# Kernel tuning notes

Hardware: AMD Instinct MI355X
Metric: run time of the kernel (lower is better)

## Reference

```python
import jax, jax.numpy as jnp
import numpy as np

TEMPERATURE_F = 0.5  # temperature_f from __init__


def setup_inputs() -> dict:
    key = jax.random.key(0)
    k1, k2 = jax.random.split(key)
    B, D = 4096, 512
    h_i = jax.random.normal(k1, (B, D), dtype=jnp.float32)
    h_j = jax.random.normal(k2, (B, D), dtype=jnp.float32)
    return {"h_i": h_i, "h_j": h_j}


def reference(h_i, h_j) -> jnp.ndarray:
    # NT-Xent loss (forward_private). N = 2*batch_size.
    B = h_i.shape[0]
    N = 2 * B
    h = jnp.concatenate([h_i, h_j], axis=0)          # [N, D]
    sim = (h @ h.T) / TEMPERATURE_F                   # [N, N]

    # Positive pairs: sim[i, i+B] and sim[i+B, i]
    sim_i_j = jnp.diagonal(sim, offset=B)             # [B]
    sim_j_i = jnp.diagonal(sim, offset=-B)            # [B]
    pos = jnp.concatenate([sim_i_j, sim_j_i], axis=0)  # [N]

    # Original builds logits = [pos | negatives] where negatives are the row of
    # sim with the diagonal and the positive entry removed, and labels are 0.
    # Cross-entropy per row = -pos_i + logsumexp(pos_i, negatives_i)
    #                       = -pos_i + logsumexp over row i of sim excluding the
    #                         diagonal (the positive entry equals pos_i, so the
    #                         set of logsumexp'd values is identical).
    neg_inf = jnp.finfo(sim.dtype).min
    diag = jnp.eye(N, dtype=bool)
    sim_masked = jnp.where(diag, neg_inf, sim)        # exclude self-similarity
    lse = jax.nn.logsumexp(sim_masked, axis=1)        # [N]

    loss = jnp.sum(lse - pos) / N                     # CE sum reduction, / N
    return loss
```

## Files before the change

### kernel.cpp

```cpp
#include <hip/hip_runtime.h>
#include <hip/hip_bf16.h>
#include <float.h>

#define BN_ 4096
#define DD  512
#define NN  8192
#define SCALE 2.0f

typedef unsigned short u16;
typedef __attribute__((ext_vector_type(8))) short short8;
typedef __attribute__((ext_vector_type(4))) float floatx4;

struct alignas(8) U16x4 { u16 x, y, z, w; };

__device__ __forceinline__ u16 f2bf(float f) {
    union { float f; unsigned u; } c; c.f = f;
    unsigned u = c.u;
    unsigned r = (u + 0x7fffu + ((u >> 16) & 1u)) >> 16;
    return (u16)r;
}

__device__ __forceinline__ void async_copy16(const u16* g, u16* l) {
    __builtin_amdgcn_global_load_lds(
        (const __attribute__((address_space(1))) void*)g,
        (__attribute__((address_space(3))) void*)l, 16, 0, 0);
}

__global__ __launch_bounds__(256) void convert_pos_kernel(const float* __restrict__ hi,
                                                          const float* __restrict__ hj,
                                                          u16* __restrict__ H,
                                                          float* __restrict__ Pos,
                                                          float* __restrict__ out) {
    __shared__ float red[4];
    int t = blockIdx.x * 256 + threadIdx.x;
    int e = t * 4;
    const int BD = BN_ * DD;
    float4 a = *(const float4*)(hi + e);
    float4 b = *(const float4*)(hj + e);
    U16x4 oa, ob;
    oa.x = f2bf(a.x); oa.y = f2bf(a.y); oa.z = f2bf(a.z); oa.w = f2bf(a.w);
    ob.x = f2bf(b.x); ob.y = f2bf(b.y); ob.z = f2bf(b.z); ob.w = f2bf(b.w);
    *(U16x4*)(H + e) = oa;
    *(U16x4*)(H + BD + e) = ob;
    float dot = a.x * b.x + a.y * b.y + a.z * b.z + a.w * b.w;
#pragma unroll
    for (int msk = 1; msk < 64; msk <<= 1) dot += __shfl_xor(dot, msk);
    int lane = threadIdx.x & 63, wid = threadIdx.x >> 6;
    if (lane == 0) red[wid] = dot;
    __syncthreads();
    if (threadIdx.x == 0) {
        Pos[blockIdx.x] = red[0] + red[1] + red[2] + red[3];
        if (blockIdx.x == 0) *out = 0.0f;
    }
}

__global__ __launch_bounds__(256, 3) void gram_kernel(const u16* __restrict__ H,
                                                      float* __restrict__ Mpart,
                                                      float* __restrict__ Spart) {
    __shared__ u16 As[128 * 64];
    __shared__ u16 Bs[128 * 64];
    __shared__ float Rm[2][128], Rs[2][128];
    __shared__ float Cm[2][128], Cs[2][128];

    const int tid  = threadIdx.x;
    const int lane = tid & 63;
    const int wid  = tid >> 6;
    const int quad = lane >> 4;
    const int ln15 = lane & 15;
    const int wr = wid >> 1, wc = wid & 1;

    int t = blockIdx.x;
    int bi = (int)((sqrtf(8.0f * (float)t + 1.0f) - 1.0f) * 0.5f);
    while ((bi + 1) * (bi + 2) / 2 <= t) bi++;
    while (bi * (bi + 1) / 2 > t) bi--;
    const int bj = t - bi * (bi + 1) / 2;
    const bool diag = (bi == bj);
    const int biBase = bi * 128, bjBase = bj * 128;

    const u16* srcA[4];
    int ldsOff[4];
#pragma unroll
    for (int j = 0; j < 4; j++) {
        int c   = j * 256 + tid;
        int row = c >> 3;
        int kc  = (c & 7) ^ (row & 7);
        srcA[j]   = H + (size_t)(biBase + row) * DD + kc * 8;
        ldsOff[j] = c * 8;
    }
    const ptrdiff_t dB = (ptrdiff_t)(bjBase - biBase) * DD;

    floatx4 acc[4][4];
#pragma unroll
    for (int i = 0; i < 4; i++)
#pragma unroll
        for (int j = 0; j < 4; j++) acc[i][j] = (floatx4)0.0f;

    for (int k0 = 0; k0 < DD; k0 += 64) {
#pragma unroll
        for (int j = 0; j < 4; j++) async_copy16(srcA[j] + k0,      &As[ldsOff[j]]);
#pragma unroll
        for (int j = 0; j < 4; j++) async_copy16(srcA[j] + dB + k0, &Bs[ldsOff[j]]);
        __syncthreads();

#pragma unroll
        for (int kk = 0; kk < 2; kk++) {
            int ck = kk * 4 + quad;
            short8 a[4], b[4];
#pragma unroll
            for (int tm = 0; tm < 4; tm++) {
                int r = wr * 64 + tm * 16 + ln15;
                a[tm] = *(const short8*)&As[(r * 8 + (ck ^ (r & 7))) * 8];
            }
#pragma unroll
            for (int tn = 0; tn < 4; tn++) {
                int r = wc * 64 + tn * 16 + ln15;
                b[tn] = *(const short8*)&Bs[(r * 8 + (ck ^ (r & 7))) * 8];
            }
#pragma unroll
            for (int tm = 0; tm < 4; tm++)
#pragma unroll
                for (int tn = 0; tn < 4; tn++)
                    acc[tm][tn] = __builtin_amdgcn_mfma_f32_16x16x32_bf16(
                        a[tm], b[tn], acc[tm][tn], 0, 0, 0);
        }
        __syncthreads();
    }

#pragma unroll
    for (int tm = 0; tm < 4; tm++)
#pragma unroll
        for (int tn = 0; tn < 4; tn++)
#pragma unroll
            for (int r = 0; r < 4; r++) {
                float v = SCALE * acc[tm][tn][r];
                if (diag) {
                    int lrow = wr * 64 + tm * 16 + quad * 4 + r;
                    int lcol = wc * 64 + tn * 16 + ln15;
                    if (lrow == lcol) v = -FLT_MAX;
                }
                acc[tm][tn][r] = v;
            }

#pragma unroll
    for (int tm = 0; tm < 4; tm++) {
#pragma unroll
        for (int r = 0; r < 4; r++) {
            float vmax = -FLT_MAX;
#pragma unroll
            for (int tn = 0; tn < 4; tn++) vmax = fmaxf(vmax, acc[tm][tn][r]);
#pragma unroll
            for (int msk = 1; msk < 16; msk <<= 1)
                vmax = fmaxf(vmax, __shfl_xor(vmax, msk));
            float s = 0.0f;
#pragma unroll
            for (int tn = 0; tn < 4; tn++) s += __expf(acc[tm][tn][r] - vmax);
#pragma unroll
            for (int msk = 1; msk < 16; msk <<= 1) s += __shfl_xor(s, msk);
            if (ln15 == 0) {
                int x = wr * 64 + tm * 16 + quad * 4 + r;
                Rm[wc][x] = vmax; Rs[wc][x] = s;
            }
        }
    }

    if (!diag) {
#pragma unroll
        for (int tn = 0; tn < 4; tn++) {
            float cm = -FLT_MAX;
#pragma unroll
            for (int tm = 0; tm < 4; tm++)
#pragma unroll
                for (int r = 0; r < 4; r++) cm = fmaxf(cm, acc[tm][tn][r]);
            cm = fmaxf(cm, __shfl_xor(cm, 16));
            cm = fmaxf(cm, __shfl_xor(cm, 32));
            float s = 0.0f;
#pragma unroll
            for (int tm = 0; tm < 4; tm++)
#pragma unroll
                for (int r = 0; r < 4; r++) s += __expf(acc[tm][tn][r] - cm);
            s += __shfl_xor(s, 16);
            s += __shfl_xor(s, 32);
            if (quad == 0) {
                int y = wc * 64 + tn * 16 + ln15;
                Cm[wr][y] = cm; Cs[wr][y] = s;
            }
        }
    }
    __syncthreads();

    if (tid < 128) {
        float m0 = Rm[0][tid], m1 = Rm[1][tid];
        float s0 = Rs[0][tid], s1 = Rs[1][tid];
        float m = fmaxf(m0, m1);
        float s = s0 * __expf(m0 - m) + s1 * __expf(m1 - m);
        Mpart[(size_t)bj * NN + biBase + tid] = m;
        Spart[(size_t)bj * NN + biBase + tid] = s;
    } else if (!diag) {
        int y = tid - 128;
        float m0 = Cm[0][y], m1 = Cm[1][y];
        float s0 = Cs[0][y], s1 = Cs[1][y];
        float m = fmaxf(m0, m1);
        float s = s0 * __expf(m0 - m) + s1 * __expf(m1 - m);
        Mpart[(size_t)bi * NN + bjBase + y] = m;
        Spart[(size_t)bi * NN + bjBase + y] = s;
    }
}

__global__ __launch_bounds__(256) void lse_kernel(const float* __restrict__ Mpart,
                                                  const float* __restrict__ Spart,
                                                  const float* __restrict__ Pos,
                                                  float* __restrict__ out) {
    __shared__ float red[256];
    int tid = threadIdx.x;
    int r = blockIdx.x * 256 + tid;
    float m = -FLT_MAX, s = 0.0f;
#pragma unroll 8
    for (int c = 0; c < 64; c++) {
        float mc = Mpart[(size_t)c * NN + r];
        float sc = Spart[(size_t)c * NN + r];
        float mn = fmaxf(m, mc);
        s = s * __expf(m - mn) + sc * __expf(mc - mn);
        m = mn;
    }
    float v = m + logf(s);
    if (tid < 64) v += -4.0f * Pos[blockIdx.x * 64 + tid];
    red[tid] = v;
    __syncthreads();
    for (int st = 128; st > 0; st >>= 1) {
        if (tid < st) red[tid] += red[tid + st];
        __syncthreads();
    }
    if (tid == 0) atomicAdd(out, red[0] * (1.0f / (float)NN));
}

extern "C" void kernel_launch(void* const* d_in, const int* in_sizes, int n_in,
                              void* d_out, int out_size, void* d_ws, size_t ws_size,
                              hipStream_t stream) {
    const float* hi = (const float*)d_in[0];
    const float* hj = (const float*)d_in[1];
    float* out = (float*)d_out;

    u16*   H     = (u16*)d_ws;
    float* Mpart = (float*)((char*)d_ws + (size_t)8 * 1024 * 1024);
    float* Spart = (float*)((char*)d_ws + (size_t)10 * 1024 * 1024);
    float* Pos   = (float*)((char*)d_ws + (size_t)12 * 1024 * 1024);

    convert_pos_kernel<<<2048, 256, 0, stream>>>(hi, hj, H, Pos, out);

    gram_kernel<<<2080, 256, 0, stream>>>(H, Mpart, Spart);

    lse_kernel<<<32, 256, 0, stream>>>(Mpart, Spart, Pos, out);
}
```

Measured before the change: 127.1 us.

## Enlarge Gram tiles to 256x256 with double-buffered async LDS pipeline

The Gram kernel switches from 128x128 tiles with 256 threads to 256x256 tiles with 512 threads (8 waves), so the triangular grid drops from 2080 to 528 blocks. Operands are double-buffered in LDS and prefetched with async global-to-LDS copies interleaved with MFMA phases, using explicit vmcnt waits, barriers and setprio. The aim is better operand reuse and less exposed load latency. The LSE kernel now splits its partial reduction across 4 waves per row group, giving more blocks. The costs are higher register pressure (32 accumulators per lane), fewer blocks for load balancing, and a fragile hand-written wait/barrier schedule.

Result: slower. 158.6 us (+24.8%).

```diff
diff --git a/kernel.cpp b/kernel.cpp
--- a/kernel.cpp
+++ b/kernel.cpp
@@ -6,6 +6,7 @@
 #define DD  512
 #define NN  8192
 #define SCALE 2.0f
+#define BUF 16384
 
 typedef unsigned short u16;
 typedef __attribute__((ext_vector_type(8))) short short8;
@@ -54,20 +55,58 @@
     }
 }
 
-__global__ __launch_bounds__(256, 3) void gram_kernel(const u16* __restrict__ H,
+#define LD8(buf, kk, off) (*(const short8*)&(buf)[(kk) * 8192 + (off)])
+#define MFMA_(va, vb, c) __builtin_amdgcn_mfma_f32_16x16x32_bf16(va, vb, c, 0, 0, 0)
+
+#define MF_ROW(mi, areg)                       \
+    acc[mi][0] = MFMA_(areg, b0, acc[mi][0]);  \
+    acc[mi][1] = MFMA_(areg, b1, acc[mi][1]);  \
+    acc[mi][2] = MFMA_(areg, b2, acc[mi][2]);  \
+    acc[mi][3] = MFMA_(areg, b3, acc[mi][3]);
+
+#define STAGE2(srcp, dstp) {                   \
+    async_copy16((srcp) + s0, (dstp) + d0);    \
+    async_copy16((srcp) + s1, (dstp) + d1); }
+
+#define PHASE(kk, mh, RB, STG)                                   \
+    {                                                            \
+        short8 a0 = LD8(cA, kk, offA[(mh)*4 + 0]);               \
+        short8 a1 = LD8(cA, kk, offA[(mh)*4 + 1]);               \
+        short8 a2 = LD8(cA, kk, offA[(mh)*4 + 2]);               \
+        short8 a3 = LD8(cA, kk, offA[(mh)*4 + 3]);               \
+        if (RB) {                                                \
+            b0 = LD8(cB, kk, offB[0]);                           \
+            b1 = LD8(cB, kk, offB[1]);                           \
+            b2 = LD8(cB, kk, offB[2]);                           \
+            b3 = LD8(cB, kk, offB[3]);                           \
+        }                                                        \
+        STG;                                                     \
+        asm volatile("s_waitcnt vmcnt(8)" ::: "memory");         \
+        __builtin_amdgcn_s_barrier();                            \
+        asm volatile("" ::: "memory");                           \
+        __builtin_amdgcn_s_setprio(1);                           \
+        MF_ROW((mh)*4 + 0, a0)                                   \
+        MF_ROW((mh)*4 + 1, a1)                                   \
+        MF_ROW((mh)*4 + 2, a2)                                   \
+        MF_ROW((mh)*4 + 3, a3)                                   \
+        __builtin_amdgcn_s_setprio(0);                           \
+        __builtin_amdgcn_s_barrier();                            \
+        asm volatile("" ::: "memory");                           \
+    }
+
+__global__ __launch_bounds__(512, 2) void gram_kernel(const u16* __restrict__ H,
                                                       float* __restrict__ Mpart,
                                                       float* __restrict__ Spart) {
-    __shared__ u16 As[128 * 64];
-    __shared__ u16 Bs[128 * 64];
-    __shared__ float Rm[2][128], Rs[2][128];
-    __shared__ float Cm[2][128], Cs[2][128];
+    __shared__ u16 As[2 * BUF];
+    __shared__ u16 Bs[2 * BUF];
 
     const int tid  = threadIdx.x;
     const int lane = tid & 63;
     const int wid  = tid >> 6;
     const int quad = lane >> 4;
     const int ln15 = lane & 15;
-    const int wr = wid >> 1, wc = wid & 1;
+    const int wr = wid >> 2;
+    const int wc = wid & 3;
 
     int t = blockIdx.x;
     int bi = (int)((sqrtf(8.0f * (float)t + 1.0f) - 1.0f) * 0.5f);
@@ -75,133 +114,139 @@
     while (bi * (bi + 1) / 2 > t) bi--;
     const int bj = t - bi * (bi + 1) / 2;
     const bool diag = (bi == bj);
-    const int biBase = bi * 128, bjBase = bj * 128;
-
-    const u16* srcA[4];
-    int ldsOff[4];
-#pragma unroll
-    for (int j = 0; j < 4; j++) {
-        int c   = j * 256 + tid;
-        int row = c >> 3;
-        int kc  = (c & 7) ^ (row & 7);
-        srcA[j]   = H + (size_t)(biBase + row) * DD + kc * 8;
-        ldsOff[j] = c * 8;
-    }
-    const ptrdiff_t dB = (ptrdiff_t)(bjBase - biBase) * DD;
-
-    floatx4 acc[4][4];
-#pragma unroll
-    for (int i = 0; i < 4; i++)
+    const int biBase = bi * 256, bjBase = bj * 256;
+
+    const u16* __restrict__ HA = H + (size_t)biBase * DD;
+    const u16* __restrict__ HB = H + (size_t)bjBase * DD;
+
+    const int c0 = tid,       r0 = c0 >> 2, p0 = c0 & 3;
+    const int c1 = 512 + tid, r1 = c1 >> 2, p1 = c1 & 3;
+    const int s0 = r0 * DD + ((p0 ^ (r0 & 3)) * 8), d0 = c0 * 8;
+    const int s1 = r1 * DD + ((p1 ^ (r1 & 3)) * 8), d1 = c1 * 8;
+
+    int offA[8], offB[4];
+#pragma unroll
+    for (int m = 0; m < 8; m++) {
+        int r = wr * 128 + m * 16 + ln15;
+        offA[m] = (r * 4 + (quad ^ (r & 3))) * 8;
+    }
+#pragma unroll
+    for (int n = 0; n < 4; n++) {
+        int r = wc * 64 + n * 16 + ln15;
+        offB[n] = (r * 4 + (quad ^ (r & 3))) * 8;
+    }
+
+    floatx4 acc[8][4];
+#pragma unroll
+    for (int i = 0; i < 8; i++)
 #pragma unroll
         for (int j = 0; j < 4; j++) acc[i][j] = (floatx4)0.0f;
 
-    for (int k0 = 0; k0 < DD; k0 += 64) {
-#pragma unroll
-        for (int j = 0; j < 4; j++) async_copy16(srcA[j] + k0,      &As[ldsOff[j]]);
-#pragma unroll
-        for (int j = 0; j < 4; j++) async_copy16(srcA[j] + dB + k0, &Bs[ldsOff[j]]);
-        __syncthreads();
-
-#pragma unroll
-        for (int kk = 0; kk < 2; kk++) {
-            int ck = kk * 4 + quad;
-            short8 a[4], b[4];
-#pragma unroll
-            for (int tm = 0; tm < 4; tm++) {
-                int r = wr * 64 + tm * 16 + ln15;
-                a[tm] = *(const short8*)&As[(r * 8 + (ck ^ (r & 7))) * 8];
-            }
-#pragma unroll
-            for (int tn = 0; tn < 4; tn++) {
-                int r = wc * 64 + tn * 16 + ln15;
-                b[tn] = *(const short8*)&Bs[(r * 8 + (ck ^ (r & 7))) * 8];
-            }
-#pragma unroll
-            for (int tm = 0; tm < 4; tm++)
-#pragma unroll
-                for (int tn = 0; tn < 4; tn++)
-                    acc[tm][tn] = __builtin_amdgcn_mfma_f32_16x16x32_bf16(
-                        a[tm], b[tn], acc[tm][tn], 0, 0, 0);
-        }
-        __syncthreads();
-    }
-
-#pragma unroll
-    for (int tm = 0; tm < 4; tm++)
-#pragma unroll
-        for (int tn = 0; tn < 4; tn++)
-#pragma unroll
-            for (int r = 0; r < 4; r++) {
-                float v = SCALE * acc[tm][tn][r];
+    STAGE2(HA,      &As[0]);
+    STAGE2(HA + 32, &As[8192]);
+    STAGE2(HB,      &Bs[0]);
+    STAGE2(HB + 32, &Bs[8192]);
+    STAGE2(HA + 64, &As[BUF]);
+    STAGE2(HB + 64, &Bs[BUF]);
+    asm volatile("s_waitcnt vmcnt(4)" ::: "memory");
+    __builtin_amdgcn_s_barrier();
+    asm volatile("" ::: "memory");
+
+#pragma unroll 2
+    for (int kt = 0; kt < 8; ++kt) {
+        u16* cA = &As[(kt & 1) * BUF];
+        u16* cB = &Bs[(kt & 1) * BUF];
+        u16* nA = &As[((kt + 1) & 1) * BUF];
+        u16* nB = &Bs[((kt + 1) & 1) * BUF];
+        const int kn1 = (kt + 1) * 64, kn2 = (kt + 2) * 64;
+        short8 b0, b1, b2, b3;
+        PHASE(0, 0, 1, if (kt < 7) STAGE2(HA + kn1 + 32, nA + 8192))
+        PHASE(0, 1, 0, if (kt < 7) STAGE2(HB + kn1 + 32, nB + 8192))
+        PHASE(1, 0, 1, if (kt < 6) STAGE2(HA + kn2,      cA))
+        PHASE(1, 1, 0, if (kt < 6) STAGE2(HB + kn2,      cB))
+    }
+
+    asm volatile("s_waitcnt vmcnt(0)" ::: "memory");
+    __syncthreads();
+
+#pragma unroll
+    for (int m = 0; m < 8; m++)
+#pragma unroll
+        for (int n = 0; n < 4; n++)
+#pragma unroll
+            for (int g = 0; g < 4; g++) {
+                float v = SCALE * acc[m][n][g];
                 if (diag) {
-                    int lrow = wr * 64 + tm * 16 + quad * 4 + r;
-                    int lcol = wc * 64 + tn * 16 + ln15;
+                    int lrow = wr * 128 + m * 16 + quad * 4 + g;
+                    int lcol = wc * 64 + n * 16 + ln15;
                     if (lrow == lcol) v = -FLT_MAX;
                 }
-                acc[tm][tn][r] = v;
+                acc[m][n][g] = v;
             }
 
-#pragma unroll
-    for (int tm = 0; tm < 4; tm++) {
-#pragma unroll
-        for (int r = 0; r < 4; r++) {
-            float vmax = -FLT_MAX;
-#pragma unroll
-            for (int tn = 0; tn < 4; tn++) vmax = fmaxf(vmax, acc[tm][tn][r]);
+    float* Rm = (float*)&As[0];
+    float* Rs = Rm + 1024;
+    float* Cm = Rs + 1024;
+    float* Cs = Cm + 512;
+
+#pragma unroll
+    for (int m = 0; m < 8; m++) {
+#pragma unroll
+        for (int g = 0; g < 4; g++) {
+            float vmax = fmaxf(fmaxf(acc[m][0][g], acc[m][1][g]),
+                               fmaxf(acc[m][2][g], acc[m][3][g]));
 #pragma unroll
             for (int msk = 1; msk < 16; msk <<= 1)
                 vmax = fmaxf(vmax, __shfl_xor(vmax, msk));
-            float s = 0.0f;
-#pragma unroll
-            for (int tn = 0; tn < 4; tn++) s += __expf(acc[tm][tn][r] - vmax);
+            float s = __expf(acc[m][0][g] - vmax) + __expf(acc[m][1][g] - vmax)
+                    + __expf(acc[m][2][g] - vmax) + __expf(acc[m][3][g] - vmax);
 #pragma unroll
             for (int msk = 1; msk < 16; msk <<= 1) s += __shfl_xor(s, msk);
             if (ln15 == 0) {
-                int x = wr * 64 + tm * 16 + quad * 4 + r;
-                Rm[wc][x] = vmax; Rs[wc][x] = s;
+                int x = wr * 128 + m * 16 + quad * 4 + g;
+                Rm[wc * 256 + x] = vmax; Rs[wc * 256 + x] = s;
             }
         }
     }
 
     if (!diag) {
 #pragma unroll
-        for (int tn = 0; tn < 4; tn++) {
+        for (int n = 0; n < 4; n++) {
             float cm = -FLT_MAX;
 #pragma unroll
-            for (int tm = 0; tm < 4; tm++)
-#pragma unroll
-                for (int r = 0; r < 4; r++) cm = fmaxf(cm, acc[tm][tn][r]);
+            for (int m = 0; m < 8; m++)
+#pragma unroll
+                for (int g = 0; g < 4; g++) cm = fmaxf(cm, acc[m][n][g]);
             cm = fmaxf(cm, __shfl_xor(cm, 16));
             cm = fmaxf(cm, __shfl_xor(cm, 32));
             float s = 0.0f;
 #pragma unroll
-            for (int tm = 0; tm < 4; tm++)
-#pragma unroll
-                for (int r = 0; r < 4; r++) s += __expf(acc[tm][tn][r] - cm);
+            for (int m = 0; m < 8; m++)
+#pragma unroll
+                for (int g = 0; g < 4; g++) s += __expf(acc[m][n][g] - cm);
             s += __shfl_xor(s, 16);
             s += __shfl_xor(s, 32);
             if (quad == 0) {
-                int y = wc * 64 + tn * 16 + ln15;
-                Cm[wr][y] = cm; Cs[wr][y] = s;
+                int y = wc * 64 + n * 16 + ln15;
+                Cm[wr * 256 + y] = cm; Cs[wr * 256 + y] = s;
             }
         }
     }
     __syncthreads();
 
-    if (tid < 128) {
-        float m0 = Rm[0][tid], m1 = Rm[1][tid];
-        float s0 = Rs[0][tid], s1 = Rs[1][tid];
-        float m = fmaxf(m0, m1);
-        float s = s0 * __expf(m0 - m) + s1 * __expf(m1 - m);
-        Mpart[(size_t)bj * NN + biBase + tid] = m;
+    if (tid < 256) {
+        float m0 = Rm[tid], m1 = Rm[256 + tid], m2 = Rm[512 + tid], m3 = Rm[768 + tid];
+        float mm = fmaxf(fmaxf(m0, m1), fmaxf(m2, m3));
+        float s = Rs[tid] * __expf(m0 - mm) + Rs[256 + tid] * __expf(m1 - mm)
+                + Rs[512 + tid] * __expf(m2 - mm) + Rs[768 + tid] * __expf(m3 - mm);
+        Mpart[(size_t)bj * NN + biBase + tid] = mm;
         Spart[(size_t)bj * NN + biBase + tid] = s;
     } else if (!diag) {
-        int y = tid - 128;
-        float m0 = Cm[0][y], m1 = Cm[1][y];
-        float s0 = Cs[0][y], s1 = Cs[1][y];
-        float m = fmaxf(m0, m1);
-        float s = s0 * __expf(m0 - m) + s1 * __expf(m1 - m);
-        Mpart[(size_t)bi * NN + bjBase + y] = m;
+        int y = tid - 256;
+        float m0 = Cm[y], m1 = Cm[256 + y];
+        float mm = fmaxf(m0, m1);
+        float s = Cs[y] * __expf(m0 - mm) + Cs[256 + y] * __expf(m1 - mm);
+        Mpart[(size_t)bi * NN + bjBase + y] = mm;
         Spart[(size_t)bi * NN + bjBase + y] = s;
     }
 }
@@ -210,20 +255,32 @@
                                                   const float* __restrict__ Spart,
                                                   const float* __restrict__ Pos,
                                                   float* __restrict__ out) {
+    __shared__ float sm[4][64], ss[4][64];
     __shared__ float red[256];
     int tid = threadIdx.x;
-    int r = blockIdx.x * 256 + tid;
+    int wid = tid >> 6, lane = tid & 63;
+    int r = blockIdx.x * 64 + lane;
     float m = -FLT_MAX, s = 0.0f;
-#pragma unroll 8
-    for (int c = 0; c < 64; c++) {
+#pragma unroll
+    for (int i = 0; i < 8; i++) {
+        int c = wid * 8 + i;
         float mc = Mpart[(size_t)c * NN + r];
         float sc = Spart[(size_t)c * NN + r];
         float mn = fmaxf(m, mc);
         s = s * __expf(m - mn) + sc * __expf(mc - mn);
         m = mn;
     }
-    float v = m + logf(s);
-    if (tid < 64) v += -4.0f * Pos[blockIdx.x * 64 + tid];
+    sm[wid][lane] = m; ss[wid][lane] = s;
+    __syncthreads();
+    float v = 0.0f;
+    if (tid < 64) {
+        float m0 = sm[0][tid], m1 = sm[1][tid], m2 = sm[2][tid], m3 = sm[3][tid];
+        float mm = fmaxf(fmaxf(m0, m1), fmaxf(m2, m3));
+        float sa = ss[0][tid] * __expf(m0 - mm) + ss[1][tid] * __expf(m1 - mm)
+                 + ss[2][tid] * __expf(m2 - mm) + ss[3][tid] * __expf(m3 - mm);
+        v = mm + logf(sa);
+        if (tid < 16) v += -4.0f * Pos[blockIdx.x * 16 + tid];
+    }
     red[tid] = v;
     __syncthreads();
     for (int st = 128; st > 0; st >>= 1) {
@@ -247,7 +304,7 @@
 
     convert_pos_kernel<<<2048, 256, 0, stream>>>(hi, hj, H, Pos, out);
 
-    gram_kernel<<<2080, 256, 0, stream>>>(H, Mpart, Spart);
-
-    lse_kernel<<<32, 256, 0, stream>>>(Mpart, Spart, Pos, out);
-}
+    gram_kernel<<<528, 512, 0, stream>>>(H, Mpart, Spart);
+
+    lse_kernel<<<128, 256, 0, stream>>>(Mpart, Spart, Pos, out);
+}
```

## Fuse LSE reduction into gram kernel via last-blocks ticket, reuse LDS, remap tiles

Applied to the files above, without the earlier changes.

Removes the separate lse_kernel launch: each gram block takes an atomic ticket when done, and the last 32 blocks spin until every tile has finished, then perform the cross-tile logsumexp merge and the final atomic accumulation. The reduction scratch arrays now alias the As/Bs tile buffers to cut LDS use, and launch bounds rise from 3 to 4 blocks per CU. Block-to-tile mapping is permuted with stride 8, presumably to spread work across XCDs. The spin-wait relies on all earlier-ticketed blocks being resident or already finished, and it makes the last blocks idle while they wait.

Result: slower. 291.6 us (+129.5%).

```diff
diff --git a/kernel.cpp b/kernel.cpp
--- a/kernel.cpp
+++ b/kernel.cpp
@@ -6,6 +6,8 @@
 #define DD  512
 #define NN  8192
 #define SCALE 2.0f
+#define NTILE 2080
+#define NDUTY 32
 
 typedef unsigned short u16;
 typedef __attribute__((ext_vector_type(8))) short short8;
@@ -30,7 +32,8 @@
                                                           const float* __restrict__ hj,
                                                           u16* __restrict__ H,
                                                           float* __restrict__ Pos,
-                                                          float* __restrict__ out) {
+                                                          float* __restrict__ out,
+                                                          unsigned* __restrict__ ticket) {
     __shared__ float red[4];
     int t = blockIdx.x * 256 + threadIdx.x;
     int e = t * 4;
@@ -50,17 +53,24 @@
     __syncthreads();
     if (threadIdx.x == 0) {
         Pos[blockIdx.x] = red[0] + red[1] + red[2] + red[3];
-        if (blockIdx.x == 0) *out = 0.0f;
-    }
-}
-
-__global__ __launch_bounds__(256, 3) void gram_kernel(const u16* __restrict__ H,
+        if (blockIdx.x == 0) { *out = 0.0f; *ticket = 0u; }
+    }
+}
+
+__global__ __launch_bounds__(256, 4) void gram_kernel(const u16* __restrict__ H,
                                                       float* __restrict__ Mpart,
-                                                      float* __restrict__ Spart) {
+                                                      float* __restrict__ Spart,
+                                                      const float* __restrict__ Pos,
+                                                      float* __restrict__ out,
+                                                      unsigned* __restrict__ ticket) {
     __shared__ u16 As[128 * 64];
     __shared__ u16 Bs[128 * 64];
-    __shared__ float Rm[2][128], Rs[2][128];
-    __shared__ float Cm[2][128], Cs[2][128];
+
+    float* Rm = (float*)&As[0];
+    float* Rs = Rm + 256;
+    float* Cm = Rs + 256;
+    float* Cs = Cm + 256;
+    unsigned* shT = (unsigned*)&Bs[0];
 
     const int tid  = threadIdx.x;
     const int lane = tid & 63;
@@ -69,7 +79,8 @@
     const int ln15 = lane & 15;
     const int wr = wid >> 1, wc = wid & 1;
 
-    int t = blockIdx.x;
+    int t = ((int)blockIdx.x & 7) * (NTILE / 8) + ((int)blockIdx.x >> 3);
+
     int bi = (int)((sqrtf(8.0f * (float)t + 1.0f) - 1.0f) * 0.5f);
     while ((bi + 1) * (bi + 2) / 2 <= t) bi++;
     while (bi * (bi + 1) / 2 > t) bi--;
@@ -158,7 +169,7 @@
             for (int msk = 1; msk < 16; msk <<= 1) s += __shfl_xor(s, msk);
             if (ln15 == 0) {
                 int x = wr * 64 + tm * 16 + quad * 4 + r;
-                Rm[wc][x] = vmax; Rs[wc][x] = s;
+                Rm[wc * 128 + x] = vmax; Rs[wc * 128 + x] = s;
             }
         }
     }
@@ -182,55 +193,63 @@
             s += __shfl_xor(s, 32);
             if (quad == 0) {
                 int y = wc * 64 + tn * 16 + ln15;
-                Cm[wr][y] = cm; Cs[wr][y] = s;
+                Cm[wr * 128 + y] = cm; Cs[wr * 128 + y] = s;
             }
         }
     }
     __syncthreads();
 
     if (tid < 128) {
-        float m0 = Rm[0][tid], m1 = Rm[1][tid];
-        float s0 = Rs[0][tid], s1 = Rs[1][tid];
+        float m0 = Rm[tid], m1 = Rm[128 + tid];
+        float s0 = Rs[tid], s1 = Rs[128 + tid];
         float m = fmaxf(m0, m1);
         float s = s0 * __expf(m0 - m) + s1 * __expf(m1 - m);
         Mpart[(size_t)bj * NN + biBase + tid] = m;
         Spart[(size_t)bj * NN + biBase + tid] = s;
     } else if (!diag) {
         int y = tid - 128;
-        float m0 = Cm[0][y], m1 = Cm[1][y];
-        float s0 = Cs[0][y], s1 = Cs[1][y];
+        float m0 = Cm[y], m1 = Cm[128 + y];
+        float s0 = Cs[y], s1 = Cs[128 + y];
         float m = fmaxf(m0, m1);
         float s = s0 * __expf(m0 - m) + s1 * __expf(m1 - m);
         Mpart[(size_t)bi * NN + bjBase + y] = m;
         Spart[(size_t)bi * NN + bjBase + y] = s;
     }
-}
-
-__global__ __launch_bounds__(256) void lse_kernel(const float* __restrict__ Mpart,
-                                                  const float* __restrict__ Spart,
-                                                  const float* __restrict__ Pos,
-                                                  float* __restrict__ out) {
-    __shared__ float red[256];
-    int tid = threadIdx.x;
-    int r = blockIdx.x * 256 + tid;
-    float m = -FLT_MAX, s = 0.0f;
+
+    __threadfence();
+    __syncthreads();
+    if (tid == 0) shT[0] = atomicAdd(ticket, 1u);
+    __syncthreads();
+    const unsigned myTicket = shT[0];
+    if (myTicket >= (unsigned)(NTILE - NDUTY)) {
+        if (tid == 0) {
+            while (atomicAdd(ticket, 0u) < (unsigned)NTILE)
+                __builtin_amdgcn_s_sleep(2);
+        }
+        __syncthreads();
+        __threadfence();
+        const int idx = (int)myTicket - (NTILE - NDUTY);
+        int r = idx * 256 + tid;
+        float m = -FLT_MAX, s = 0.0f;
 #pragma unroll 8
-    for (int c = 0; c < 64; c++) {
-        float mc = Mpart[(size_t)c * NN + r];
-        float sc = Spart[(size_t)c * NN + r];
-        float mn = fmaxf(m, mc);
-        s = s * __expf(m - mn) + sc * __expf(mc - mn);
-        m = mn;
-    }
-    float v = m + logf(s);
-    if (tid < 64) v += -4.0f * Pos[blockIdx.x * 64 + tid];
-    red[tid] = v;
-    __syncthreads();
-    for (int st = 128; st > 0; st >>= 1) {
-        if (tid < st) red[tid] += red[tid + st];
-        __syncthreads();
-    }
-    if (tid == 0) atomicAdd(out, red[0] * (1.0f / (float)NN));
+        for (int c = 0; c < 64; c++) {
+            float mc = Mpart[(size_t)c * NN + r];
+            float sc = Spart[(size_t)c * NN + r];
+            float mn = fmaxf(m, mc);
+            s = s * __expf(m - mn) + sc * __expf(mc - mn);
+            m = mn;
+        }
+        float v = m + logf(s);
+        if (tid < 64) v += -4.0f * Pos[idx * 64 + tid];
+        float* red = (float*)&As[0];
+        red[tid] = v;
+        __syncthreads();
+        for (int st = 128; st > 0; st >>= 1) {
+            if (tid < st) red[tid] += red[tid + st];
+            __syncthreads();
+        }
+        if (tid == 0) atomicAdd(out, red[0] * (1.0f / (float)NN));
+    }
 }
 
 extern "C" void kernel_launch(void* const* d_in, const int* in_sizes, int n_in,
@@ -240,14 +259,13 @@
     const float* hj = (const float*)d_in[1];
     float* out = (float*)d_out;
 
-    u16*   H     = (u16*)d_ws;
-    float* Mpart = (float*)((char*)d_ws + (size_t)8 * 1024 * 1024);
-    float* Spart = (float*)((char*)d_ws + (size_t)10 * 1024 * 1024);
-    float* Pos   = (float*)((char*)d_ws + (size_t)12 * 1024 * 1024);
-
-    convert_pos_kernel<<<2048, 256, 0, stream>>>(hi, hj, H, Pos, out);
-
-    gram_kernel<<<2080, 256, 0, stream>>>(H, Mpart, Spart);
-
-    lse_kernel<<<32, 256, 0, stream>>>(Mpart, Spart, Pos, out);
-}
+    u16*      H      = (u16*)d_ws;
+    float*    Mpart  = (float*)((char*)d_ws + (size_t)8 * 1024 * 1024);
+    float*    Spart  = (float*)((char*)d_ws + (size_t)10 * 1024 * 1024);
+    float*    Pos    = (float*)((char*)d_ws + (size_t)12 * 1024 * 1024);
+    unsigned* ticket = (unsigned*)((char*)d_ws + (size_t)13 * 1024 * 1024);
+
+    convert_pos_kernel<<<2048, 256, 0, stream>>>(hi, hj, H, Pos, out, ticket);
+
+    gram_kernel<<<NTILE, 256, 0, stream>>>(H, Mpart, Spart, Pos, out, ticket);
+}
```

## Raise gram occupancy, alias reduction buffers into LDS, swizzle tiles, split LSE

Applied to the files above, without the earlier changes.

The gram kernel's launch bounds rise from 3 to 4 waves per SIMD, and its row/column reduction scratch now aliases the As tile buffer, which frees LDS so more blocks fit per CU. Block indices are remapped with a stride-8 permutation, probably to spread neighbouring triangle tiles across XCDs for cache locality. The LSE kernel now splits the 64 column partials across 4 waves per row group, running 128 blocks instead of 32 to get more parallelism. Risks are register spilling under the tighter launch bound and lower L2 reuse if the tile remap interacts badly with caching.

Result: slower. 131.0 us (+3.1%).

```diff
diff --git a/kernel.cpp b/kernel.cpp
--- a/kernel.cpp
+++ b/kernel.cpp
@@ -6,6 +6,7 @@
 #define DD  512
 #define NN  8192
 #define SCALE 2.0f
+#define NTILE 2080
 
 typedef unsigned short u16;
 typedef __attribute__((ext_vector_type(8))) short short8;
@@ -54,13 +55,16 @@
     }
 }
 
-__global__ __launch_bounds__(256, 3) void gram_kernel(const u16* __restrict__ H,
+__global__ __launch_bounds__(256, 4) void gram_kernel(const u16* __restrict__ H,
                                                       float* __restrict__ Mpart,
                                                       float* __restrict__ Spart) {
     __shared__ u16 As[128 * 64];
     __shared__ u16 Bs[128 * 64];
-    __shared__ float Rm[2][128], Rs[2][128];
-    __shared__ float Cm[2][128], Cs[2][128];
+
+    float* Rm = (float*)&As[0];
+    float* Rs = Rm + 256;
+    float* Cm = Rs + 256;
+    float* Cs = Cm + 256;
 
     const int tid  = threadIdx.x;
     const int lane = tid & 63;
@@ -69,7 +73,8 @@
     const int ln15 = lane & 15;
     const int wr = wid >> 1, wc = wid & 1;
 
-    int t = blockIdx.x;
+    int t = ((int)blockIdx.x & 7) * (NTILE / 8) + ((int)blockIdx.x >> 3);
+
     int bi = (int)((sqrtf(8.0f * (float)t + 1.0f) - 1.0f) * 0.5f);
     while ((bi + 1) * (bi + 2) / 2 <= t) bi++;
     while (bi * (bi + 1) / 2 > t) bi--;
@@ -158,7 +163,7 @@
             for (int msk = 1; msk < 16; msk <<= 1) s += __shfl_xor(s, msk);
             if (ln15 == 0) {
                 int x = wr * 64 + tm * 16 + quad * 4 + r;
-                Rm[wc][x] = vmax; Rs[wc][x] = s;
+                Rm[wc * 128 + x] = vmax; Rs[wc * 128 + x] = s;
             }
         }
     }
@@ -182,23 +187,23 @@
             s += __shfl_xor(s, 32);
             if (quad == 0) {
                 int y = wc * 64 + tn * 16 + ln15;
-                Cm[wr][y] = cm; Cs[wr][y] = s;
+                Cm[wr * 128 + y] = cm; Cs[wr * 128 + y] = s;
             }
         }
     }
     __syncthreads();
 
     if (tid < 128) {
-        float m0 = Rm[0][tid], m1 = Rm[1][tid];
-        float s0 = Rs[0][tid], s1 = Rs[1][tid];
+        float m0 = Rm[tid], m1 = Rm[128 + tid];
+        float s0 = Rs[tid], s1 = Rs[128 + tid];
         float m = fmaxf(m0, m1);
         float s = s0 * __expf(m0 - m) + s1 * __expf(m1 - m);
         Mpart[(size_t)bj * NN + biBase + tid] = m;
         Spart[(size_t)bj * NN + biBase + tid] = s;
     } else if (!diag) {
         int y = tid - 128;
-        float m0 = Cm[0][y], m1 = Cm[1][y];
-        float s0 = Cs[0][y], s1 = Cs[1][y];
+        float m0 = Cm[y], m1 = Cm[128 + y];
+        float s0 = Cs[y], s1 = Cs[128 + y];
         float m = fmaxf(m0, m1);
         float s = s0 * __expf(m0 - m) + s1 * __expf(m1 - m);
         Mpart[(size_t)bi * NN + bjBase + y] = m;
@@ -210,20 +215,32 @@
                                                   const float* __restrict__ Spart,
                                                   const float* __restrict__ Pos,
                                                   float* __restrict__ out) {
+    __shared__ float sm[4][64], ss[4][64];
     __shared__ float red[256];
     int tid = threadIdx.x;
-    int r = blockIdx.x * 256 + tid;
+    int wid = tid >> 6, lane = tid & 63;
+    int r = blockIdx.x * 64 + lane;
     float m = -FLT_MAX, s = 0.0f;
-#pragma unroll 8
-    for (int c = 0; c < 64; c++) {
+#pragma unroll
+    for (int i = 0; i < 16; i++) {
+        int c = wid * 16 + i;
         float mc = Mpart[(size_t)c * NN + r];
         float sc = Spart[(size_t)c * NN + r];
         float mn = fmaxf(m, mc);
         s = s * __expf(m - mn) + sc * __expf(mc - mn);
         m = mn;
     }
-    float v = m + logf(s);
-    if (tid < 64) v += -4.0f * Pos[blockIdx.x * 64 + tid];
+    sm[wid][lane] = m; ss[wid][lane] = s;
+    __syncthreads();
+    float v = 0.0f;
+    if (tid < 64) {
+        float m0 = sm[0][tid], m1 = sm[1][tid], m2 = sm[2][tid], m3 = sm[3][tid];
+        float mm = fmaxf(fmaxf(m0, m1), fmaxf(m2, m3));
+        float sa = ss[0][tid] * __expf(m0 - mm) + ss[1][tid] * __expf(m1 - mm)
+                 + ss[2][tid] * __expf(m2 - mm) + ss[3][tid] * __expf(m3 - mm);
+        v = mm + logf(sa);
+        if (tid < 16) v += -4.0f * Pos[blockIdx.x * 16 + tid];
+    }
     red[tid] = v;
     __syncthreads();
     for (int st = 128; st > 0; st >>= 1) {
@@ -247,7 +264,7 @@
 
     convert_pos_kernel<<<2048, 256, 0, stream>>>(hi, hj, H, Pos, out);
 
-    gram_kernel<<<2080, 256, 0, stream>>>(H, Mpart, Spart);
-
-    lse_kernel<<<32, 256, 0, stream>>>(Mpart, Spart, Pos, out);
-}
+    gram_kernel<<<NTILE, 256, 0, stream>>>(H, Mpart, Spart);
+
+    lse_kernel<<<128, 256, 0, stream>>>(Mpart, Spart, Pos, out);
+}
```
